# Performance work log

Measured on AMD Instinct MI355X. Metric: run time of the kernel, lower is better.

The kernel has to match this reference:

```python
import jax, jax.numpy as jnp
import numpy as np

NUM_HEADS = 8
HEAD_DIM = 128
MAX_RES = 224.0


def rope_embed(feat_shape, dim, max_res=MAX_RES):
    # timm pixel_freq_bands: 2**linspace(0, log2(max_res)-1, dim//4) * pi
    num_bands = dim // 4
    bands = (2.0 ** jnp.linspace(0.0, float(np.log2(max_res)) - 1.0, num_bands)) * jnp.pi
    # pixel coords in [-1, 1] per spatial dim
    coords = [jnp.linspace(-1.0, 1.0, s) for s in feat_shape]
    grid = jnp.stack(jnp.meshgrid(*coords, indexing='ij'), axis=-1)[..., None]  # [H,W,2,1]
    pos = grid * bands  # [H,W,2,num_bands]
    n = int(np.prod(feat_shape))
    sin = jnp.repeat(jnp.sin(pos).reshape(n, -1), 2, axis=-1)  # [n, dim]
    cos = jnp.repeat(jnp.cos(pos).reshape(n, -1), 2, axis=-1)  # [n, dim]
    return sin, cos


def _rot(x):
    # interleaved rotate-half: (x0,x1,x2,x3,...) -> (-x1,x0,-x3,x2,...)
    return jnp.stack([-x[..., 1::2], x[..., ::2]], axis=-1).reshape(x.shape)


def setup_inputs() -> dict:
    key = jax.random.key(0)
    k1, k2, k3, k4 = jax.random.split(key, 4)
    C, E = 1024, 1024
    x = jax.random.normal(k1, (64, C, 16, 16), dtype=jnp.float32)
    qkv_w = jax.random.normal(k2, (3 * E, C), dtype=jnp.float32) * (C ** -0.5)
    qkv_b = jnp.zeros((3 * E,), dtype=jnp.float32)
    proj_w = jax.random.normal(k3, (E, E), dtype=jnp.float32) * (E ** -0.5)
    proj_b = jax.random.normal(k4, (E,), dtype=jnp.float32) * 0.02
    return {"x": x, "qkv_w": qkv_w, "qkv_b": qkv_b, "proj_w": proj_w, "proj_b": proj_b}


def reference(x, qkv_w, qkv_b, proj_w, proj_b):
    B, C, H, W = x.shape
    n = H * W
    scale = HEAD_DIM ** -0.5
    sin_emb, cos_emb = rope_embed((H, W), HEAD_DIM)  # [n, head_dim]

    t = x.reshape(B, C, n).transpose(0, 2, 1)                      # [B, n, C]
    t = jnp.concatenate([t.mean(axis=1, keepdims=True), t], axis=1)  # [B, n+1, C]

    qkv = t @ qkv_w.T + qkv_b                                      # [B, n+1, 3E]
    qkv = qkv.reshape(B, n + 1, 3, NUM_HEADS, HEAD_DIM).transpose(2, 0, 3, 1, 4)
    q, k, v = qkv[0], qkv[1], qkv[2]                               # [B, h, n+1, d]

    def apply_rope(z):
        zc, zs = z[:, :, :1], z[:, :, 1:]
        zs = zs * cos_emb + _rot(zs) * sin_emb
        return jnp.concatenate([zc, zs], axis=2)

    q = apply_rope(q)
    k = apply_rope(k)

    attn = jax.nn.softmax(jnp.einsum('bhqd,bhkd->bhqk', q, k) * scale, axis=-1)
    out = jnp.einsum('bhqk,bhkd->bhqd', attn, v)
    out = out.transpose(0, 2, 1, 3).reshape(B, n + 1, -1)           # [B, n+1, E]
    out = out @ proj_w.T + proj_b
    return out[:, 0]
```

## Files before the change

kernel.cpp:

```cpp
#include <hip/hip_runtime.h>
#include <math.h>

#define PI_F 3.14159265358979323846f
#define KSTEP 0.21959209425992272f

using bf16x8 = __attribute__((ext_vector_type(8))) short;
using f32x4 = __attribute__((ext_vector_type(4))) float;
using u16x8 = __attribute__((ext_vector_type(8))) unsigned short;

static __device__ __forceinline__ float wave_reduce_sum(float v) {
#pragma unroll
  for (int off = 32; off; off >>= 1) v += __shfl_down(v, off);
  return v;
}

static __device__ __forceinline__ unsigned short f2bf(float f) {
  unsigned u = __float_as_uint(f);
  return (unsigned short)((u + 0x7fffu + ((u >> 16) & 1u)) >> 16);
}

static __device__ __forceinline__ float bf2f(unsigned short s) {
  return __uint_as_float(((unsigned)s) << 16);
}

static __device__ __forceinline__ void gload_lds16(const void* g, void* l) {
  __builtin_amdgcn_global_load_lds((const __attribute__((address_space(1))) unsigned int*)g,
                                   (__attribute__((address_space(3))) unsigned int*)l, 16, 0, 0);
}

__global__ __launch_bounds__(256) void prep_kernel(const float* __restrict__ x,
                                                   const float* __restrict__ qkv_w,
                                                   const float* __restrict__ qkv_b,
                                                   unsigned short* __restrict__ xt,
                                                   float* __restrict__ t_mean,
                                                   unsigned short* __restrict__ wkT,
                                                   float2* __restrict__ sc) {
  const int bid = blockIdx.x;
  const int t = threadIdx.x;
  __shared__ float tile[64 * 33];
  __shared__ float tl2[64 * 65];
  if (bid < 1024) {
    const int ct = bid & 15, b = bid >> 4;
    const int cl = t >> 2, pq = (t & 3) * 8;
    const int pl = t >> 3, cq = (t & 7) * 8;
    float sum = 0.0f;
    const float* xrow = x + ((size_t)(b * 1024 + ct * 64 + cl) * 256) + pq;
    unsigned short* xtb = xt + (size_t)b * 262144 + ct * 64;
    for (int pt = 0; pt < 8; ++pt) {
      const float4 v0 = *reinterpret_cast<const float4*>(xrow + pt * 32);
      const float4 v1 = *reinterpret_cast<const float4*>(xrow + pt * 32 + 4);
      tile[cl * 33 + pq + 0] = v0.x; tile[cl * 33 + pq + 1] = v0.y;
      tile[cl * 33 + pq + 2] = v0.z; tile[cl * 33 + pq + 3] = v0.w;
      tile[cl * 33 + pq + 4] = v1.x; tile[cl * 33 + pq + 5] = v1.y;
      tile[cl * 33 + pq + 6] = v1.z; tile[cl * 33 + pq + 7] = v1.w;
      sum += (v0.x + v0.y) + (v0.z + v0.w) + (v1.x + v1.y) + (v1.z + v1.w);
      __syncthreads();
      u16x8 o;
#pragma unroll
      for (int e = 0; e < 8; ++e) o[e] = f2bf(tile[(cq + e) * 33 + pl]);
      *reinterpret_cast<u16x8*>(xtb + (size_t)(pt * 32 + pl) * 1024 + cq) = o;
      __syncthreads();
    }
    sum += __shfl_xor(sum, 1);
    sum += __shfl_xor(sum, 2);
    if ((t & 3) == 0) t_mean[b * 1024 + ct * 64 + cl] = sum * (1.0f / 256.0f);
  } else if (bid < 1280) {
    const int bb = bid - 1024;
    const int h = bb >> 5, t5 = bb & 31;
    const int dt = t5 >> 4, ct = t5 & 15;
    {
      const int dl = t >> 2, cq = (t & 3) * 16;
      const float* src = qkv_w + (size_t)(1024 + h * 128 + dt * 64 + dl) * 1024 + ct * 64 + cq;
#pragma unroll
      for (int i = 0; i < 4; ++i) {
        const float4 v = *reinterpret_cast<const float4*>(src + i * 4);
        tl2[dl * 65 + cq + i * 4 + 0] = v.x; tl2[dl * 65 + cq + i * 4 + 1] = v.y;
        tl2[dl * 65 + cq + i * 4 + 2] = v.z; tl2[dl * 65 + cq + i * 4 + 3] = v.w;
      }
    }
    __syncthreads();
    {
      const int cl = t >> 2, dq = (t & 3) * 16;
      unsigned short* dst = wkT + (size_t)(h * 1152 + ct * 64 + cl) * 128 + dt * 64 + dq;
      u16x8 o0, o1;
#pragma unroll
      for (int e = 0; e < 8; ++e) {
        o0[e] = f2bf(tl2[(dq + e) * 65 + cl]);
        o1[e] = f2bf(tl2[(dq + 8 + e) * 65 + cl]);
      }
      *reinterpret_cast<u16x8*>(dst) = o0;
      *reinterpret_cast<u16x8*>(dst + 8) = o1;
    }
  } else {
    const int idx = (bid - 1280) * 256 + t;
    const int m = idx >> 8, j = idx & 255;
    const float band = exp2f((float)(m & 31) * KSTEP) * PI_F;
    const float coord = (m < 32) ? (-1.0f + (2.0f / 15.0f) * (float)(j >> 4))
                                 : (-1.0f + (2.0f / 15.0f) * (float)(j & 15));
    float sn, cs;
    sincosf(coord * band, &sn, &cs);
    sc[idx] = make_float2(sn, cs);
  }
}

__global__ __launch_bounds__(256) void gemm_splitk(
    const float* __restrict__ A, int lda, int aStrideZ,
    const float* __restrict__ B, int ldb, int bStrideZ,
    float* __restrict__ Cp, int ldc, int cStrideZ, int cStrideKc, int KC) {
  const int nt = blockIdx.x, mt = blockIdx.y;
  const int z = blockIdx.z / KC, kc = blockIdx.z % KC;
  const int tid = threadIdx.x;
  A += (size_t)z * aStrideZ + (size_t)mt * 32 * lda + kc * 256;
  B += (size_t)z * bStrideZ + (size_t)nt * 64 * ldb + kc * 256;
  Cp += (size_t)kc * cStrideKc + (size_t)z * cStrideZ + (size_t)mt * 32 * ldc + nt * 64;

  __shared__ float As[32][34];
  __shared__ float Bs[32][68];

  const int tm = tid >> 4;
  const int tn = tid & 15;
  float acc0[4] = {0, 0, 0, 0}, acc1[4] = {0, 0, 0, 0};

  for (int k0 = 0; k0 < 256; k0 += 32) {
    {
      const int m = tid >> 3, kq = tid & 7;
      float4 v = *reinterpret_cast<const float4*>(A + (size_t)m * lda + k0 + kq * 4);
      As[kq * 4 + 0][m] = v.x; As[kq * 4 + 1][m] = v.y;
      As[kq * 4 + 2][m] = v.z; As[kq * 4 + 3][m] = v.w;
    }
#pragma unroll
    for (int r = 0; r < 2; ++r) {
      const int idx = r * 256 + tid;
      const int n = idx >> 3, kq = idx & 7;
      float4 v = *reinterpret_cast<const float4*>(B + (size_t)n * ldb + k0 + kq * 4);
      Bs[kq * 4 + 0][n] = v.x; Bs[kq * 4 + 1][n] = v.y;
      Bs[kq * 4 + 2][n] = v.z; Bs[kq * 4 + 3][n] = v.w;
    }
    __syncthreads();
#pragma unroll
    for (int k = 0; k < 32; ++k) {
      const float a0 = As[k][tm * 2], a1 = As[k][tm * 2 + 1];
      const float4 bb = *reinterpret_cast<const float4*>(&Bs[k][tn * 4]);
      acc0[0] += a0 * bb.x; acc0[1] += a0 * bb.y; acc0[2] += a0 * bb.z; acc0[3] += a0 * bb.w;
      acc1[0] += a1 * bb.x; acc1[1] += a1 * bb.y; acc1[2] += a1 * bb.z; acc1[3] += a1 * bb.w;
    }
    __syncthreads();
  }
  *reinterpret_cast<float4*>(Cp + (size_t)(tm * 2) * ldc + tn * 4) =
      make_float4(acc0[0], acc0[1], acc0[2], acc0[3]);
  *reinterpret_cast<float4*>(Cp + (size_t)(tm * 2 + 1) * ldc + tn * 4) =
      make_float4(acc1[0], acc1[1], acc1[2], acc1[3]);
}

__global__ __launch_bounds__(256) void gemm_proj_splitk(
    const float* __restrict__ Apart, const float* __restrict__ abias,
    const float* __restrict__ B, float* __restrict__ Cp) {
  const int nt = blockIdx.x, mt = blockIdx.y, kc = blockIdx.z;
  const int tid = threadIdx.x;
  B += (size_t)nt * 64 * 1024 + kc * 256;
  Cp += (size_t)kc * 65536 + (size_t)mt * 32 * 1024 + nt * 64;

  __shared__ float As[32][34];
  __shared__ float Bs[32][68];

  const int tm = tid >> 4;
  const int tn = tid & 15;
  float acc0[4] = {0, 0, 0, 0}, acc1[4] = {0, 0, 0, 0};

  for (int k0 = 0; k0 < 256; k0 += 32) {
    {
      const int m = tid >> 3, kq = tid & 7;
      const int kg = kc * 256 + k0 + kq * 4;
      const float* Ab = Apart + (size_t)(mt * 32 + m) * 1024 + kg;
      float4 v = *reinterpret_cast<const float4*>(abias + kg);
#pragma unroll
      for (int r = 0; r < 4; ++r) {
        const float4 p = *reinterpret_cast<const float4*>(Ab + (size_t)r * 65536);
        v.x += p.x; v.y += p.y; v.z += p.z; v.w += p.w;
      }
      As[kq * 4 + 0][m] = v.x; As[kq * 4 + 1][m] = v.y;
      As[kq * 4 + 2][m] = v.z; As[kq * 4 + 3][m] = v.w;
    }
#pragma unroll
    for (int r = 0; r < 2; ++r) {
      const int idx = r * 256 + tid;
      const int n = idx >> 3, kq = idx & 7;
      float4 v = *reinterpret_cast<const float4*>(B + (size_t)n * 1024 + k0 + kq * 4);
      Bs[kq * 4 + 0][n] = v.x; Bs[kq * 4 + 1][n] = v.y;
      Bs[kq * 4 + 2][n] = v.z; Bs[kq * 4 + 3][n] = v.w;
    }
    __syncthreads();
#pragma unroll
    for (int k = 0; k < 32; ++k) {
      const float a0 = As[k][tm * 2], a1 = As[k][tm * 2 + 1];
      const float4 bb = *reinterpret_cast<const float4*>(&Bs[k][tn * 4]);
      acc0[0] += a0 * bb.x; acc0[1] += a0 * bb.y; acc0[2] += a0 * bb.z; acc0[3] += a0 * bb.w;
      acc1[0] += a1 * bb.x; acc1[1] += a1 * bb.y; acc1[2] += a1 * bb.z; acc1[3] += a1 * bb.w;
    }
    __syncthreads();
  }
  *reinterpret_cast<float4*>(Cp + (size_t)(tm * 2) * 1024 + tn * 4) =
      make_float4(acc0[0], acc0[1], acc0[2], acc0[3]);
  *reinterpret_cast<float4*>(Cp + (size_t)(tm * 2 + 1) * 1024 + tn * 4) =
      make_float4(acc1[0], acc1[1], acc1[2], acc1[3]);
}

__global__ __launch_bounds__(256) void reduce4_bias(const float* __restrict__ part,
                                                    const float* __restrict__ bias,
                                                    float* __restrict__ out) {
  const int i = blockIdx.x * 256 + threadIdx.x;
  out[i] = part[i] + part[i + 65536] + part[i + 131072] + part[i + 196608] + bias[i & 1023];
}

__global__ __launch_bounds__(512, 4) void scores_u(
    const unsigned short* __restrict__ wkT, const unsigned short* __restrict__ xt,
    const float* __restrict__ q0p, const float* __restrict__ qkv_b,
    const float2* __restrict__ sc, const float* __restrict__ t_mean,
    float* __restrict__ u) {
  const int l = blockIdx.x;
  const int b = ((l >> 5) << 3) | (l & 7);
  const int ht = (l >> 3) & 3;
  const int tid = threadIdx.x;
  const int w = tid >> 6, lane = tid & 63;
  const int rgrp = lane >> 4;

  const int hh_ = (w & 3) >> 1, sgen = (w & 3) & 1, ctl = w >> 2;

  __shared__ __align__(16) char smem[74240];
  float* persist = reinterpret_cast<float*>(smem + 69632);
  float* q0l = persist;
  float* k0l = persist + 256;
  float* biasg = persist + 512;
  float* ps = persist + 576;
  float* smax = persist + 580;
  float* ssum = persist + 588;
  float* attnl = persist + 596;
  char* Btile = smem + 65536;

  const unsigned short* xtb = xt + (size_t)b * 262144;

#define STAGE_A(buf, c0)                                                        \
  {                                                                             \
    char* Ab_ = smem + (buf)*16384;                                             \
    _Pragma("unroll") for (int i = 0; i < 2; ++i) {                             \
      const int row_ = w * 32 + i * 16 + (lane >> 2);                           \
      const int sl_ = ((lane & 3) ^ ((row_ >> 1) & 3)) * 8;                     \
      gload_lds16(xtb + (size_t)row_ * 1024 + (c0) + sl_,                       \
                  Ab_ + (w * 2 + i) * 1024);                                    \
    }                                                                           \
  }
#define STAGE_W(buf, c0)                                                        \
  {                                                                             \
    char* Wb_ = smem + 32768 + (buf)*16384;                                     \
    _Pragma("unroll") for (int i = 0; i < 2; ++i) {                             \
      const int r_ = (w * 2 + i) * 4 + rgrp;                        \
      const int c_ = r_ & 31;                                                   \
      const int L_ = lane & 15;                                                 \
      const int so_ = (L_ >> 3) * 64 + ((L_ & 7) ^ ((c_ >> 1) & 7)) * 8;        \
      gload_lds16(wkT + ((size_t)(ht * 2 + (r_ >> 5)) * 1152 + (c0) + c_) * 128 \
                      + so_,                                                    \
                  Wb_ + (w * 2 + i) * 1024);                                    \
    }                                                                           \
  }

  STAGE_A(0, 0);
  STAGE_W(0, 0);
  if (tid < 256) {
    const float* qp = q0p + (size_t)b * 2048 + ht * 256 + tid;
    q0l[tid] = qkv_b[ht * 256 + tid] + qp[0] + qp[131072] + qp[262144] + qp[393216];
    const float* kp = qp + 1024;
    k0l[tid] = qkv_b[1024 + ht * 256 + tid] + kp[0] + kp[131072] + kp[262144] + kp[393216];
  }
  __syncthreads();

  bf16x8 rq[2];
  {
    const int v = lane & 15;
    const int jrep = sgen ? v : v * 16;
#pragma unroll
    for (int kk = 0; kk < 2; ++kk) {
#pragma unroll
      for (int e = 0; e < 8; e += 2) {
        const int d = kk * 32 + rgrp * 8 + e;
        const int p = d >> 1;
        const float qe = q0l[hh_ * 128 + sgen * 64 + 2 * p];
        const float qo = q0l[hh_ * 128 + sgen * 64 + 2 * p + 1];
        const float2 tt = sc[(sgen * 32 + p) * 256 + jrep];
        rq[kk][e] = (short)f2bf(qe * tt.y + qo * tt.x);
        rq[kk][e + 1] = (short)f2bf(qo * tt.y - qe * tt.x);
      }
    }
  }

  f32x4 acc[2][4] = {};
  for (int t = 0; t < 32; ++t) {
    {
      const int src = (t + 1 > 31) ? 31 : (t + 1);
      STAGE_A((t + 1) & 1, src * 32);
      STAGE_W((t + 1) & 1, src * 32);
    }
    asm volatile("s_waitcnt vmcnt(4)" ::: "memory");
    __builtin_amdgcn_s_barrier();
    const char* Ab = smem + (t & 1) * 16384;
    const char* Wb = smem + 32768 + (t & 1) * 16384;
    {
      f32x4 accg = {};
#pragma unroll
      for (int kk = 0; kk < 2; ++kk) {
        const int c_ = ctl * 16 + (lane & 15);
        const int slot = sgen * 8 + ((kk * 4 + rgrp) ^ ((c_ >> 1) & 7));
        const bf16x8 wf = *reinterpret_cast<const bf16x8*>(
            Wb + (hh_ * 32 + c_) * 256 + (slot << 4));
        accg = __builtin_amdgcn_mfma_f32_16x16x32_bf16(wf, rq[kk], accg, 0, 0, 0);
      }
      const int n = (w & 3) * 16 + (lane & 15);
      const int cslot = ctl * 2 + (rgrp >> 1);
      const unsigned u0 = (unsigned)f2bf(accg[0]) | ((unsigned)f2bf(accg[1]) << 16);
      const unsigned u1 = (unsigned)f2bf(accg[2]) | ((unsigned)f2bf(accg[3]) << 16);
      *reinterpret_cast<uint2*>(Btile + n * 64 + ((cslot ^ ((n >> 1) & 3)) << 4) +
                                (rgrp & 1) * 8) = make_uint2(u0, u1);
    }
    asm volatile("s_waitcnt lgkmcnt(0)" ::: "memory");
    __builtin_amdgcn_s_barrier();
    {
      bf16x8 af[2], bfr[4];
#pragma unroll
      for (int mi = 0; mi < 2; ++mi) {
        const int row = w * 32 + mi * 16 + (lane & 15);
        const int slot = rgrp ^ ((row >> 1) & 3);
        af[mi] = *reinterpret_cast<const bf16x8*>(Ab + row * 64 + (slot << 4));
      }
#pragma unroll
      for (int ni = 0; ni < 4; ++ni) {
        const int n = ni * 16 + (lane & 15);
        const int slot = rgrp ^ ((n >> 1) & 3);
        bfr[ni] = *reinterpret_cast<const bf16x8*>(Btile + n * 64 + (slot << 4));
      }
      __builtin_amdgcn_s_setprio(1);
#pragma unroll
      for (int mi = 0; mi < 2; ++mi)
#pragma unroll
        for (int ni = 0; ni < 4; ++ni)
          acc[mi][ni] =
              __builtin_amdgcn_mfma_f32_16x16x32_bf16(af[mi], bfr[ni], acc[mi][ni], 0, 0, 0);
      __builtin_amdgcn_s_setprio(0);
    }
    __builtin_amdgcn_s_barrier();
    asm volatile("" ::: "memory");
  }
#undef STAGE_A
#undef STAGE_W

  asm volatile("s_waitcnt vmcnt(0)" ::: "memory");
  __syncthreads();

  float* Sp = reinterpret_cast<float*>(smem);
  float* up2 = reinterpret_cast<float*>(smem + 16384);

#pragma unroll
  for (int mi = 0; mi < 2; ++mi)
#pragma unroll
    for (int ni = 0; ni < 4; ++ni)
#pragma unroll
      for (int rr = 0; rr < 4; ++rr) {
        const int j = w * 32 + mi * 16 + (rgrp << 2) + rr;
        const int col = ni * 16 + (lane & 15);
        const int s = (col >> 4) & 1;
        const int sel = s ? (j & 15) : (j >> 4);
        if ((col & 15) == sel) Sp[(j * 2 + (col >> 5)) * 2 + s] = acc[mi][ni][rr];
      }
  if (tid < 64) {
    const int h_ = tid >> 5, s_ = (tid >> 4) & 1, v_ = tid & 15;
    const float* bk = qkv_b + 1024 + (ht * 2 + h_) * 128 + s_ * 64;
    const int jrep = s_ ? v_ : v_ * 16;
    float a = 0.0f;
#pragma unroll 4
    for (int p = 0; p < 32; ++p) {
      const float qe = q0l[h_ * 128 + s_ * 64 + 2 * p];
      const float qo = q0l[h_ * 128 + s_ * 64 + 2 * p + 1];
      const float2 tt = sc[(s_ * 32 + p) * 256 + jrep];
      a += (qe * tt.y + qo * tt.x) * bk[2 * p] + (qo * tt.y - qe * tt.x) * bk[2 * p + 1];
    }
    biasg[tid] = a;
  }
  if (tid < 256) {
    float pr = q0l[tid] * k0l[tid];
    pr = wave_reduce_sum(pr);
    if (lane == 0) ps[w] = pr;
  }
  __syncthreads();

  const float scale = 0.08838834764831845f;
  float e0 = 0.0f, e1 = 0.0f, eb0 = 0.0f, eb1 = 0.0f;
  if (tid < 256) {
    const float va0 = scale * (Sp[tid * 4 + 0] + Sp[tid * 4 + 1] + biasg[tid >> 4] +
                               biasg[16 + (tid & 15)]);
    const float va1 = scale * (Sp[tid * 4 + 2] + Sp[tid * 4 + 3] + biasg[32 + (tid >> 4)] +
                               biasg[48 + (tid & 15)]);
    float vb0 = -3.0e38f, vb1 = -3.0e38f;
    if (tid == 0) {
      vb0 = scale * (ps[0] + ps[1]);
      vb1 = scale * (ps[2] + ps[3]);
    }
    float m0 = fmaxf(va0, vb0), m1 = fmaxf(va1, vb1);
#pragma unroll
    for (int off = 32; off; off >>= 1) {
      m0 = fmaxf(m0, __shfl_xor(m0, off));
      m1 = fmaxf(m1, __shfl_xor(m1, off));
    }
    if (lane == 0) { smax[w] = m0; smax[4 + w] = m1; }
  }
  __syncthreads();
  if (tid < 256) {
    const float g0 = fmaxf(fmaxf(smax[0], smax[1]), fmaxf(smax[2], smax[3]));
    const float g1 = fmaxf(fmaxf(smax[4], smax[5]), fmaxf(smax[6], smax[7]));
    const float va0 = scale * (Sp[tid * 4 + 0] + Sp[tid * 4 + 1] + biasg[tid >> 4] +
                               biasg[16 + (tid & 15)]);
    const float va1 = scale * (Sp[tid * 4 + 2] + Sp[tid * 4 + 3] + biasg[32 + (tid >> 4)] +
                               biasg[48 + (tid & 15)]);
    e0 = expf(va0 - g0);
    e1 = expf(va1 - g1);
    if (tid == 0) {
      eb0 = expf(scale * (ps[0] + ps[1]) - g0);
      eb1 = expf(scale * (ps[2] + ps[3]) - g1);
    }
    float s0 = e0 + eb0, s1 = e1 + eb1;
#pragma unroll
    for (int off = 32; off; off >>= 1) {
      s0 += __shfl_xor(s0, off);
      s1 += __shfl_xor(s1, off);
    }
    if (lane == 0) { ssum[w] = s0; ssum[4 + w] = s1; }
  }
  __syncthreads();
  if (tid < 256) {
    const float inv0 = 1.0f / (ssum[0] + ssum[1] + ssum[2] + ssum[3]);
    const float inv1 = 1.0f / (ssum[4] + ssum[5] + ssum[6] + ssum[7]);
    attnl[1 + tid] = e0 * inv0;
    attnl[257 + 1 + tid] = e1 * inv1;
    if (tid == 0) { attnl[0] = eb0 * inv0; attnl[257] = eb1 * inv1; }
  }
  __syncthreads();

  {
    const int jh = w >> 2, cq = w & 3;
    const int c0 = cq * 256 + lane * 4;
    float ua0[4] = {}, ua1[4] = {};
    const unsigned short* xr = xtb + c0;
    for (int jj = 0; jj < 128; ++jj) {
      const int j = jh * 128 + jj;
      const float a0 = attnl[1 + j];
      const float a1 = attnl[258 + j];
      const ushort4 v = *reinterpret_cast<const ushort4*>(xr + (size_t)j * 1024);
      const float xs[4] = {bf2f(v.x), bf2f(v.y), bf2f(v.z), bf2f(v.w)};
#pragma unroll
      for (int e = 0; e < 4; ++e) {
        ua0[e] += a0 * xs[e];
        ua1[e] += a1 * xs[e];
      }
    }
#pragma unroll
    for (int e = 0; e < 4; ++e) {
      up2[jh * 2048 + 0 * 1024 + c0 + e] = ua0[e];
      up2[jh * 2048 + 1 * 1024 + c0 + e] = ua1[e];
    }
  }
  __syncthreads();
#pragma unroll
  for (int r = 0; r < 4; ++r) {
    const int o = tid * 4 + r;
    const int h2 = o >> 10, c = o & 1023;
    float s = up2[h2 * 1024 + c] + up2[2048 + h2 * 1024 + c];
    s += attnl[h2 * 257] * t_mean[b * 1024 + c];
    u[((size_t)b * 8 + ht * 2 + h2) * 1024 + c] = s;
  }
}

extern "C" void kernel_launch(void* const* d_in, const int* in_sizes, int n_in,
                              void* d_out, int out_size, void* d_ws, size_t ws_size,
                              hipStream_t stream) {
  const float* x = (const float*)d_in[0];
  const float* qkv_w = (const float*)d_in[1];
  const float* qkv_b = (const float*)d_in[2];
  const float* proj_w = (const float*)d_in[3];
  const float* proj_b = (const float*)d_in[4];
  float* out = (float*)d_out;

  float* ws = (float*)d_ws;
  float* t_mean = ws;
  float* q0k0_part = ws + 65536;
  float* u = ws + 589824;
  float* out0_part = ws + 1114112;
  float* out_part = ws + 1376256;
  float2* sc = (float2*)(ws + 1638400);
  unsigned short* wkT = (unsigned short*)(ws + 1671168);
  unsigned short* x_t = (unsigned short*)(ws + 11698176);

  prep_kernel<<<1344, 256, 0, stream>>>(x, qkv_w, qkv_b, x_t, t_mean, wkT, sc);

  gemm_splitk<<<dim3(32, 2, 4), 256, 0, stream>>>(t_mean, 1024, 0, qkv_w, 1024, 0,
                                                  q0k0_part, 2048, 0, 131072, 4);

  scores_u<<<256, 512, 0, stream>>>(wkT, x_t, q0k0_part, qkv_b, sc, t_mean, u);

  gemm_splitk<<<dim3(2, 2, 32), 256, 0, stream>>>(u, 8192, 1024,
                                                  qkv_w + (size_t)2048 * 1024, 1024, 131072,
                                                  out0_part, 1024, 128, 65536, 4);

  gemm_proj_splitk<<<dim3(16, 2, 4), 256, 0, stream>>>(out0_part, qkv_b + 2048, proj_w, out_part);

  reduce4_bias<<<256, 256, 0, stream>>>(out_part, proj_b, out);
}
```

Measured before the change: 101.3 us.

## Load scores_u operands directly to registers with prefetch instead of LDS staging

```diff
diff --git a/kernel.cpp b/kernel.cpp
--- a/kernel.cpp
+++ b/kernel.cpp
@@ -21,11 +21,6 @@
 
 static __device__ __forceinline__ float bf2f(unsigned short s) {
   return __uint_as_float(((unsigned)s) << 16);
-}
-
-static __device__ __forceinline__ void gload_lds16(const void* g, void* l) {
-  __builtin_amdgcn_global_load_lds((const __attribute__((address_space(1))) unsigned int*)g,
-                                   (__attribute__((address_space(3))) unsigned int*)l, 16, 0, 0);
 }
 
 __global__ __launch_bounds__(256) void prep_kernel(const float* __restrict__ x,
@@ -212,7 +207,7 @@
   out[i] = part[i] + part[i + 65536] + part[i + 131072] + part[i + 196608] + bias[i & 1023];
 }
 
-__global__ __launch_bounds__(512, 4) void scores_u(
+__global__ __launch_bounds__(512) void scores_u(
     const unsigned short* __restrict__ wkT, const unsigned short* __restrict__ xt,
     const float* __restrict__ q0p, const float* __restrict__ qkv_b,
     const float2* __restrict__ sc, const float* __restrict__ t_mean,
@@ -226,8 +221,8 @@
 
   const int hh_ = (w & 3) >> 1, sgen = (w & 3) & 1, ctl = w >> 2;
 
-  __shared__ __align__(16) char smem[74240];
-  float* persist = reinterpret_cast<float*>(smem + 69632);
+  __shared__ __align__(16) char smem[33792];
+  float* persist = reinterpret_cast<float*>(smem);
   float* q0l = persist;
   float* k0l = persist + 256;
   float* biasg = persist + 512;
@@ -235,36 +230,11 @@
   float* smax = persist + 580;
   float* ssum = persist + 588;
   float* attnl = persist + 596;
-  char* Btile = smem + 65536;
+  char* Bt0 = smem + 4864;
+  char* Bt1 = smem + 8960;
 
   const unsigned short* xtb = xt + (size_t)b * 262144;
 
-#define STAGE_A(buf, c0)                                                        \
-  {                                                                             \
-    char* Ab_ = smem + (buf)*16384;                                             \
-    _Pragma("unroll") for (int i = 0; i < 2; ++i) {                             \
-      const int row_ = w * 32 + i * 16 + (lane >> 2);                           \
-      const int sl_ = ((lane & 3) ^ ((row_ >> 1) & 3)) * 8;                     \
-      gload_lds16(xtb + (size_t)row_ * 1024 + (c0) + sl_,                       \
-                  Ab_ + (w * 2 + i) * 1024);                                    \
-    }                                                                           \
-  }
-#define STAGE_W(buf, c0)                                                        \
-  {                                                                             \
-    char* Wb_ = smem + 32768 + (buf)*16384;                                     \
-    _Pragma("unroll") for (int i = 0; i < 2; ++i) {                             \
-      const int r_ = (w * 2 + i) * 4 + rgrp;                        \
-      const int c_ = r_ & 31;                                                   \
-      const int L_ = lane & 15;                                                 \
-      const int so_ = (L_ >> 3) * 64 + ((L_ & 7) ^ ((c_ >> 1) & 7)) * 8;        \
-      gload_lds16(wkT + ((size_t)(ht * 2 + (r_ >> 5)) * 1152 + (c0) + c_) * 128 \
-                      + so_,                                                    \
-                  Wb_ + (w * 2 + i) * 1024);                                    \
-    }                                                                           \
-  }
-
-  STAGE_A(0, 0);
-  STAGE_W(0, 0);
   if (tid < 256) {
     const float* qp = q0p + (size_t)b * 2048 + ht * 256 + tid;
     q0l[tid] = qkv_b[ht * 256 + tid] + qp[0] + qp[131072] + qp[262144] + qp[393216];
@@ -292,70 +262,93 @@
     }
   }
 
+  const int c_ = ctl * 16 + (lane & 15);
+  const unsigned short* wrow =
+      wkT + ((size_t)(ht * 2 + hh_) * 1152 + c_) * 128 + sgen * 64 + rgrp * 8;
+  const unsigned short* arow0 = xtb + (size_t)(w * 32 + (lane & 15)) * 1024 + rgrp * 8;
+  const unsigned short* arow1 = arow0 + 16 * 1024;
+
+#define WLOAD(dst0, dst1, tt)                                                   \
+  {                                                                             \
+    const unsigned short* p_ = wrow + (size_t)(tt)*4096;                        \
+    dst0 = *reinterpret_cast<const bf16x8*>(p_);                                \
+    dst1 = *reinterpret_cast<const bf16x8*>(p_ + 32);                           \
+  }
+#define ALOAD(dst0, dst1, tt)                                                   \
+  {                                                                             \
+    dst0 = *reinterpret_cast<const bf16x8*>(arow0 + (tt)*32);                   \
+    dst1 = *reinterpret_cast<const bf16x8*>(arow1 + (tt)*32);                   \
+  }
+#define BGEN(W0, W1, dstBt)                                                     \
+  {                                                                             \
+    f32x4 accg = {};                                                            \
+    accg = __builtin_amdgcn_mfma_f32_16x16x32_bf16(W0, rq[0], accg, 0, 0, 0);   \
+    accg = __builtin_amdgcn_mfma_f32_16x16x32_bf16(W1, rq[1], accg, 0, 0, 0);   \
+    const int n_ = (w & 3) * 16 + (lane & 15);                                  \
+    const int cslot_ = ctl * 2 + (rgrp >> 1);                                   \
+    const unsigned u0_ =                                                        \
+        (unsigned)f2bf(accg[0]) | ((unsigned)f2bf(accg[1]) << 16);              \
+    const unsigned u1_ =                                                        \
+        (unsigned)f2bf(accg[2]) | ((unsigned)f2bf(accg[3]) << 16);              \
+    *reinterpret_cast<uint2*>((dstBt) + n_ * 64 +                               \
+                              ((cslot_ ^ ((n_ >> 1) & 3)) << 4) +               \
+                              (rgrp & 1) * 8) = make_uint2(u0_, u1_);           \
+  }
+
   f32x4 acc[2][4] = {};
+  bf16x8 af0c, af1c, af0n, af1n, wf0n, wf1n, wf0n2, wf1n2;
+  {
+    bf16x8 wf00, wf10;
+    WLOAD(wf00, wf10, 0);
+    BGEN(wf00, wf10, Bt0);
+  }
+  ALOAD(af0c, af1c, 0);
+  WLOAD(wf0n, wf1n, 1);
+  asm volatile("s_waitcnt lgkmcnt(0)" ::: "memory");
+  __builtin_amdgcn_s_barrier();
+
   for (int t = 0; t < 32; ++t) {
+    if (t < 31) {
+      char* dst = ((t + 1) & 1) ? Bt1 : Bt0;
+      BGEN(wf0n, wf1n, dst);
+    }
     {
-      const int src = (t + 1 > 31) ? 31 : (t + 1);
-      STAGE_A((t + 1) & 1, src * 32);
-      STAGE_W((t + 1) & 1, src * 32);
-    }
-    asm volatile("s_waitcnt vmcnt(4)" ::: "memory");
-    __builtin_amdgcn_s_barrier();
-    const char* Ab = smem + (t & 1) * 16384;
-    const char* Wb = smem + 32768 + (t & 1) * 16384;
+      const int ta = (t + 1 > 31) ? 31 : (t + 1);
+      const int tw = (t + 2 > 31) ? 31 : (t + 2);
+      ALOAD(af0n, af1n, ta);
+      WLOAD(wf0n2, wf1n2, tw);
+    }
     {
-      f32x4 accg = {};
-#pragma unroll
-      for (int kk = 0; kk < 2; ++kk) {
-        const int c_ = ctl * 16 + (lane & 15);
-        const int slot = sgen * 8 + ((kk * 4 + rgrp) ^ ((c_ >> 1) & 7));
-        const bf16x8 wf = *reinterpret_cast<const bf16x8*>(
-            Wb + (hh_ * 32 + c_) * 256 + (slot << 4));
-        accg = __builtin_amdgcn_mfma_f32_16x16x32_bf16(wf, rq[kk], accg, 0, 0, 0);
-      }
-      const int n = (w & 3) * 16 + (lane & 15);
-      const int cslot = ctl * 2 + (rgrp >> 1);
-      const unsigned u0 = (unsigned)f2bf(accg[0]) | ((unsigned)f2bf(accg[1]) << 16);
-      const unsigned u1 = (unsigned)f2bf(accg[2]) | ((unsigned)f2bf(accg[3]) << 16);
-      *reinterpret_cast<uint2*>(Btile + n * 64 + ((cslot ^ ((n >> 1) & 3)) << 4) +
-                                (rgrp & 1) * 8) = make_uint2(u0, u1);
-    }
-    asm volatile("s_waitcnt lgkmcnt(0)" ::: "memory");
-    __builtin_amdgcn_s_barrier();
-    {
-      bf16x8 af[2], bfr[4];
-#pragma unroll
-      for (int mi = 0; mi < 2; ++mi) {
-        const int row = w * 32 + mi * 16 + (lane & 15);
-        const int slot = rgrp ^ ((row >> 1) & 3);
-        af[mi] = *reinterpret_cast<const bf16x8*>(Ab + row * 64 + (slot << 4));
-      }
+      const char* Bb = (t & 1) ? Bt1 : Bt0;
+      bf16x8 bfr[4];
 #pragma unroll
       for (int ni = 0; ni < 4; ++ni) {
         const int n = ni * 16 + (lane & 15);
         const int slot = rgrp ^ ((n >> 1) & 3);
-        bfr[ni] = *reinterpret_cast<const bf16x8*>(Btile + n * 64 + (slot << 4));
+        bfr[ni] = *reinterpret_cast<const bf16x8*>(Bb + n * 64 + (slot << 4));
       }
       __builtin_amdgcn_s_setprio(1);
 #pragma unroll
-      for (int mi = 0; mi < 2; ++mi)
-#pragma unroll
-        for (int ni = 0; ni < 4; ++ni)
-          acc[mi][ni] =
-              __builtin_amdgcn_mfma_f32_16x16x32_bf16(af[mi], bfr[ni], acc[mi][ni], 0, 0, 0);
+      for (int ni = 0; ni < 4; ++ni) {
+        acc[0][ni] = __builtin_amdgcn_mfma_f32_16x16x32_bf16(af0c, bfr[ni], acc[0][ni], 0, 0, 0);
+        acc[1][ni] = __builtin_amdgcn_mfma_f32_16x16x32_bf16(af1c, bfr[ni], acc[1][ni], 0, 0, 0);
+      }
       __builtin_amdgcn_s_setprio(0);
     }
+    af0c = af0n; af1c = af1n;
+    wf0n = wf0n2; wf1n = wf1n2;
+    asm volatile("s_waitcnt lgkmcnt(0)" ::: "memory");
     __builtin_amdgcn_s_barrier();
     asm volatile("" ::: "memory");
   }
-#undef STAGE_A
-#undef STAGE_W
-
-  asm volatile("s_waitcnt vmcnt(0)" ::: "memory");
-  __syncthreads();
-
-  float* Sp = reinterpret_cast<float*>(smem);
-  float* up2 = reinterpret_cast<float*>(smem + 16384);
+#undef WLOAD
+#undef ALOAD
+#undef BGEN
+
+  __syncthreads();
+
+  float* Sp = reinterpret_cast<float*>(smem + 13056);
+  float* up2 = reinterpret_cast<float*>(smem + 17408);
 
 #pragma unroll
   for (int mi = 0; mi < 2; ++mi)
```

After: 102.1 us. About the same (+0.7%).
